# Performance work log

Measured on AMD Instinct MI355X. Metric: run time of the kernel, lower is better.

## Reference

```python
import jax, jax.numpy as jnp
import numpy as np

MODES = 256


def setup_inputs() -> dict:
    key = jax.random.key(0)
    k1, k2, k3, k4, k5 = jax.random.split(key, 5)
    B, C_IN, C_OUT, N, KM = 8, 128, 128, 8192, 32
    scale = 1.0 / (C_IN * C_OUT)
    return {
        "x": jax.random.normal(k1, (B, C_IN, N), dtype=jnp.float32),
        "wbases": jax.random.normal(k2, (B, N, MODES), dtype=jnp.float32),
        "bases": jax.random.normal(k3, (B, N, MODES), dtype=jnp.float32),
        "weights": scale * jax.random.normal(k4, (C_IN, C_OUT, KM), dtype=jnp.float32),
        "D": jax.random.normal(k5, (KM, MODES), dtype=jnp.float32),
    }


def reference(x, wbases, bases, weights, D):
    # Project onto weighted bases: (b, c_in, n) x (b, n, modes) -> (b, c_in, modes)
    x_hat = jnp.einsum('bcx,bxk->bck', x, wbases[:, :, :MODES])
    # D-weighted channel mixing. Original: x_hat1[b,i,j,k] = x_hat[b,i,k]*D[j,k];
    # y[b,o,k] = sum_{i,j} x_hat1[b,i,j,k] * weights[i,o,j]
    # Equivalent fused contraction (same math, no 4D broadcast):
    y_hat = jnp.einsum('bik,jk,ioj->bok', x_hat, D, weights)
    # Reconstruct on output bases: (b, c_out, modes) x (b, n, modes) -> (b, c_out, n)
    y = jnp.einsum('bck,bxk->bcx', y_hat, bases[:, :, :MODES])
    return y
```

## Files before the change

### kernel.cpp

```cpp
#include <hip/hip_runtime.h>

#define B_    8
#define CIN   128
#define COUT  128
#define NX    8192
#define KMJ   32
#define MODES 256

typedef short bf16x8 __attribute__((ext_vector_type(8)));
typedef float f32x4  __attribute__((ext_vector_type(4)));

__device__ __forceinline__ float bf2f(unsigned short u) {
    union { unsigned int i; float f; } v; v.i = ((unsigned int)u) << 16; return v.f;
}
__device__ __forceinline__ unsigned short f2bf(float f) {
    union { float f; unsigned int i; } v; v.f = f;
    unsigned int x = v.i;
    return (unsigned short)((x + 0x7fffu + ((x >> 16) & 1u)) >> 16);
}
__device__ __forceinline__ bf16x8 cvt8(const float* __restrict__ p) {
    f32x4 a = *(const f32x4*)p;
    f32x4 b = *(const f32x4*)(p + 4);
    bf16x8 r;
    r[0] = (short)f2bf(a[0]); r[1] = (short)f2bf(a[1]);
    r[2] = (short)f2bf(a[2]); r[3] = (short)f2bf(a[3]);
    r[4] = (short)f2bf(b[0]); r[5] = (short)f2bf(b[1]);
    r[6] = (short)f2bf(b[2]); r[7] = (short)f2bf(b[3]);
    return r;
}
__device__ __forceinline__ ushort4 cvt4(f32x4 a) {
    ushort4 r;
    r.x = f2bf(a[0]); r.y = f2bf(a[1]); r.z = f2bf(a[2]); r.w = f2bf(a[3]);
    return r;
}

__global__ __launch_bounds__(256) void k1_wk(const float* __restrict__ W,
                                             const float* __restrict__ D,
                                             unsigned short* __restrict__ Wk) {
    int wave = threadIdx.x >> 6, lane = threadIdx.x & 63;
    int quad = lane >> 4, l16 = lane & 15;
    int gw  = blockIdx.x * 4 + wave;
    int oi0 = gw * 16;
    int i0  = oi0 & 127, o0 = oi0 >> 7;
    bf16x8 bfrag = cvt8(W + ((size_t)(i0 + l16) * COUT + o0) * KMJ + quad * 8);
    for (int mt = 0; mt < 16; mt++) {
        int k0 = mt * 16;
        bf16x8 afrag;
#pragma unroll
        for (int jj = 0; jj < 8; jj++)
            afrag[jj] = (short)f2bf(D[(quad * 8 + jj) * MODES + k0 + l16]);
        f32x4 acc = {0.f, 0.f, 0.f, 0.f};
        acc = __builtin_amdgcn_mfma_f32_16x16x32_bf16(afrag, bfrag, acc, 0, 0, 0);
#pragma unroll
        for (int r = 0; r < 4; r++)
            Wk[(size_t)(k0 + quad * 4 + r) * (CIN * COUT) + oi0 + l16] = f2bf(acc[r]);
    }
}

__global__ __launch_bounds__(512) void k2_xhat(const float* __restrict__ X,
                                               const float* __restrict__ WB,
                                               unsigned short* __restrict__ PART) {
    __shared__ __align__(16) unsigned short Xs[128 * 40];
    __shared__ __align__(16) unsigned short WBs[32 * 260];
    int nt = blockIdx.x, b = blockIdx.y;
    int r0 = nt * 256;
    int t  = threadIdx.x;
    int wave = t >> 6, lane = t & 63;
    int wm = wave >> 2, wn = wave & 3;
    int quad = lane >> 4, l16 = lane & 15;

    const float* xb  = X  + (size_t)b * CIN * NX;
    const float* wbb = WB + (size_t)b * NX * MODES;

    int xn4 = t & 7,  xc  = t >> 3;
    int wk4 = t & 63, wn0 = t >> 6;

    f32x4 acc[4][4];
#pragma unroll
    for (int i = 0; i < 4; i++)
#pragma unroll
        for (int j = 0; j < 4; j++) acc[i][j] = (f32x4){0.f, 0.f, 0.f, 0.f};

    for (int s = 0; s < 8; s++) {
        int rs = r0 + s * 32;
        f32x4 xv0 = *(const f32x4*)(xb + (size_t)xc * NX + rs + xn4 * 4);
        f32x4 xv1 = *(const f32x4*)(xb + (size_t)(xc + 64) * NX + rs + xn4 * 4);
        f32x4 wv[4];
#pragma unroll
        for (int r = 0; r < 4; r++)
            wv[r] = *(const f32x4*)(wbb + (size_t)(rs + wn0 + 8 * r) * MODES + wk4 * 4);

        __syncthreads();
        *(ushort4*)(Xs + xc * 40 + xn4 * 4)        = cvt4(xv0);
        *(ushort4*)(Xs + (xc + 64) * 40 + xn4 * 4) = cvt4(xv1);
#pragma unroll
        for (int r = 0; r < 4; r++)
            *(ushort4*)(WBs + (wn0 + 8 * r) * 260 + wk4 * 4) = cvt4(wv[r]);
        __syncthreads();

        bf16x8 af[4];
#pragma unroll
        for (int tm = 0; tm < 4; tm++)
            af[tm] = *(const bf16x8*)(Xs + (wm * 64 + tm * 16 + l16) * 40 + quad * 8);
        bf16x8 bfv[4];
#pragma unroll
        for (int tn = 0; tn < 4; tn++) {
            int km = wn * 64 + tn * 16 + l16;
#pragma unroll
            for (int jj = 0; jj < 8; jj++)
                bfv[tn][jj] = (short)WBs[(quad * 8 + jj) * 260 + km];
        }
#pragma unroll
        for (int tm = 0; tm < 4; tm++)
#pragma unroll
            for (int tn = 0; tn < 4; tn++)
                acc[tm][tn] = __builtin_amdgcn_mfma_f32_16x16x32_bf16(af[tm], bfv[tn], acc[tm][tn], 0, 0, 0);
    }

    unsigned short* pb = PART + ((size_t)b * 32 + nt) * (CIN * MODES);
#pragma unroll
    for (int tm = 0; tm < 4; tm++) {
        int c = wm * 64 + tm * 16 + quad * 4;
#pragma unroll
        for (int tn = 0; tn < 4; tn++) {
            int km = wn * 64 + tn * 16 + l16;
#pragma unroll
            for (int r = 0; r < 4; r++)
                pb[(size_t)(c + r) * MODES + km] = f2bf(acc[tm][tn][r]);
        }
    }
}

__global__ __launch_bounds__(256) void k2b_red(const unsigned short* __restrict__ PART,
                                               float* __restrict__ XH) {
    int e0 = blockIdx.x * 1024 + threadIdx.x;
#pragma unroll
    for (int r = 0; r < 4; r++) {
        int e = e0 + r * 256;
        int b = e >> 15, rem = e & 32767;
        const unsigned short* p = PART + (size_t)b * 32 * (CIN * MODES) + rem;
        float acc = 0.f;
#pragma unroll
        for (int nt = 0; nt < 32; nt++) acc += bf2f(p[nt * (CIN * MODES)]);
        XH[e] = acc;
    }
}

__global__ __launch_bounds__(256) void k3_yhat(const float* __restrict__ XH,
                                               const unsigned short* __restrict__ Wk,
                                               unsigned short* __restrict__ YH) {
    __shared__ float xs[128][8];
    int k = blockIdx.x;
    int t = threadIdx.x;
#pragma unroll
    for (int l = 0; l < 4; l++) {
        int e = l * 256 + t;
        int i = e >> 3, b = e & 7;
        xs[i][b] = XH[(size_t)b * (CIN * MODES) + (size_t)i * MODES + k];
    }
    __syncthreads();
    int o = t & 127, bh = t >> 7;
    const unsigned short* wp = Wk + (size_t)k * (CIN * COUT) + (size_t)o * CIN;
    f32x4 acc = {0.f, 0.f, 0.f, 0.f};
    for (int ii = 0; ii < 16; ii++) {
        bf16x8 wc = *(const bf16x8*)(wp + ii * 8);
#pragma unroll
        for (int jj = 0; jj < 8; jj++) {
            float w = bf2f((unsigned short)wc[jj]);
            f32x4 xv = *(const f32x4*)&xs[ii * 8 + jj][bh * 4];
            acc += w * xv;
        }
    }
#pragma unroll
    for (int r = 0; r < 4; r++)
        YH[((size_t)(bh * 4 + r) * COUT + o) * MODES + k] = f2bf(acc[r]);
}

__global__ __launch_bounds__(256) void k4_y(const unsigned short* __restrict__ YH,
                                            const float* __restrict__ BA,
                                            float* __restrict__ Y) {
    __shared__ __align__(16) unsigned short As[128 * 32];
    __shared__ __align__(16) unsigned short Bs[128 * 32];
    int b  = blockIdx.y;
    int n0 = blockIdx.x * 128;
    int t  = threadIdx.x;
    int wave = t >> 6, lane = t & 63;
    int wm = wave >> 1, wn = wave & 1;
    int quad = lane >> 4, l16 = lane & 15;

    const unsigned short* yhb = YH + (size_t)b * COUT * MODES;
    const float* bab = BA + (size_t)b * NX * MODES + (size_t)n0 * MODES;

    int E0 = t * 8;
    int row0 = E0 >> 5, kk0 = E0 & 31;
    int row1 = (2048 + E0) >> 5, kk1 = (2048 + E0) & 31;

    f32x4 acc[4][4];
#pragma unroll
    for (int i = 0; i < 4; i++)
#pragma unroll
        for (int j = 0; j < 4; j++) acc[i][j] = (f32x4){0.f, 0.f, 0.f, 0.f};

    bf16x8 av0 = *(const bf16x8*)(yhb + (size_t)row0 * MODES + kk0);
    bf16x8 av1 = *(const bf16x8*)(yhb + (size_t)row1 * MODES + kk1);
    f32x4 bv0a = *(const f32x4*)(bab + (size_t)row0 * MODES + kk0);
    f32x4 bv0b = *(const f32x4*)(bab + (size_t)row0 * MODES + kk0 + 4);
    f32x4 bv1a = *(const f32x4*)(bab + (size_t)row1 * MODES + kk1);
    f32x4 bv1b = *(const f32x4*)(bab + (size_t)row1 * MODES + kk1 + 4);

    for (int step = 0; step < 8; step++) {
        __syncthreads();
        *(bf16x8*)(As + E0)        = av0;
        *(bf16x8*)(As + 2048 + E0) = av1;
        bf16x8 bs0, bs1;
        bs0[0]=(short)f2bf(bv0a[0]); bs0[1]=(short)f2bf(bv0a[1]);
        bs0[2]=(short)f2bf(bv0a[2]); bs0[3]=(short)f2bf(bv0a[3]);
        bs0[4]=(short)f2bf(bv0b[0]); bs0[5]=(short)f2bf(bv0b[1]);
        bs0[6]=(short)f2bf(bv0b[2]); bs0[7]=(short)f2bf(bv0b[3]);
        bs1[0]=(short)f2bf(bv1a[0]); bs1[1]=(short)f2bf(bv1a[1]);
        bs1[2]=(short)f2bf(bv1a[2]); bs1[3]=(short)f2bf(bv1a[3]);
        bs1[4]=(short)f2bf(bv1b[0]); bs1[5]=(short)f2bf(bv1b[1]);
        bs1[6]=(short)f2bf(bv1b[2]); bs1[7]=(short)f2bf(bv1b[3]);
        *(bf16x8*)(Bs + E0)        = bs0;
        *(bf16x8*)(Bs + 2048 + E0) = bs1;
        __syncthreads();

        if (step < 7) {
            int ks = (step + 1) * 32;
            av0  = *(const bf16x8*)(yhb + (size_t)row0 * MODES + ks + kk0);
            av1  = *(const bf16x8*)(yhb + (size_t)row1 * MODES + ks + kk1);
            bv0a = *(const f32x4*)(bab + (size_t)row0 * MODES + ks + kk0);
            bv0b = *(const f32x4*)(bab + (size_t)row0 * MODES + ks + kk0 + 4);
            bv1a = *(const f32x4*)(bab + (size_t)row1 * MODES + ks + kk1);
            bv1b = *(const f32x4*)(bab + (size_t)row1 * MODES + ks + kk1 + 4);
        }

        bf16x8 af[4], bfv[4];
#pragma unroll
        for (int tm = 0; tm < 4; tm++) {
            int c = wm * 64 + tm * 16 + l16;
            af[tm] = *(const bf16x8*)(As + c * 32 + quad * 8);
        }
#pragma unroll
        for (int tn = 0; tn < 4; tn++) {
            int n = wn * 64 + tn * 16 + l16;
            bfv[tn] = *(const bf16x8*)(Bs + n * 32 + quad * 8);
        }
#pragma unroll
        for (int tm = 0; tm < 4; tm++)
#pragma unroll
            for (int tn = 0; tn < 4; tn++)
                acc[tm][tn] = __builtin_amdgcn_mfma_f32_16x16x32_bf16(af[tm], bfv[tn], acc[tm][tn], 0, 0, 0);
    }

    float* yb = Y + (size_t)b * COUT * NX;
#pragma unroll
    for (int tm = 0; tm < 4; tm++) {
        int o = wm * 64 + tm * 16 + quad * 4;
#pragma unroll
        for (int tn = 0; tn < 4; tn++) {
            int n = n0 + wn * 64 + tn * 16 + l16;
#pragma unroll
            for (int r = 0; r < 4; r++)
                yb[(size_t)(o + r) * NX + n] = acc[tm][tn][r];
        }
    }
}

extern "C" void kernel_launch(void* const* d_in, const int* in_sizes, int n_in,
                              void* d_out, int out_size, void* d_ws, size_t ws_size,
                              hipStream_t stream) {
    const float* X  = (const float*)d_in[0];
    const float* WB = (const float*)d_in[1];
    const float* BA = (const float*)d_in[2];
    const float* W  = (const float*)d_in[3];
    const float* D  = (const float*)d_in[4];
    float* Y = (float*)d_out;

    char* ws = (char*)d_ws;
    unsigned short* Wk   = (unsigned short*)ws;
    float*          XH   = (float*)(ws + (8u << 20));
    unsigned short* YH   = (unsigned short*)(ws + (9u << 20));
    unsigned short* PART = (unsigned short*)(ws + (10u << 20));

    k1_wk  <<<256,          256, 0, stream>>>(W, D, Wk);
    k2_xhat<<<dim3(32, 8),  512, 0, stream>>>(X, WB, PART);
    k2b_red<<<256,          256, 0, stream>>>(PART, XH);
    k3_yhat<<<MODES,        256, 0, stream>>>(XH, Wk, YH);
    k4_y   <<<dim3(64, 8),  256, 0, stream>>>(YH, BA, Y);
}
```

Before: 221.0 us.

## Split x_hat kernel over mode halves, prefetch next tile, transpose WB in LDS

The projection kernel grid gains a third dimension that splits the 256 modes into two halves of 128. This doubles the block count from 256 to 512 for better CU occupancy, at the cost of each half re-reading x. Loads are now register-prefetched one stage ahead so global reads overlap the MFMA work, and thread roles are split between x loading and WB loading. WB is stored transposed in LDS so B fragments are read as single 16-byte vector loads instead of eight scalar strided reads.

```diff
diff --git a/kernel.cpp b/kernel.cpp
--- a/kernel.cpp
+++ b/kernel.cpp
@@ -57,70 +57,94 @@
     }
 }
 
-__global__ __launch_bounds__(512) void k2_xhat(const float* __restrict__ X,
-                                               const float* __restrict__ WB,
-                                               unsigned short* __restrict__ PART) {
+__global__ __launch_bounds__(512, 4) void k2_xhat(const float* __restrict__ X,
+                                                  const float* __restrict__ WB,
+                                                  unsigned short* __restrict__ PART) {
     __shared__ __align__(16) unsigned short Xs[128 * 40];
-    __shared__ __align__(16) unsigned short WBs[32 * 260];
-    int nt = blockIdx.x, b = blockIdx.y;
+    __shared__ __align__(16) unsigned short WBT[8 * 552];
+    int nt = blockIdx.x, b = blockIdx.y, kh = blockIdx.z;
     int r0 = nt * 256;
     int t  = threadIdx.x;
     int wave = t >> 6, lane = t & 63;
-    int wm = wave >> 2, wn = wave & 3;
+    int wm = wave >> 1, wn = wave & 1;
     int quad = lane >> 4, l16 = lane & 15;
 
     const float* xb  = X  + (size_t)b * CIN * NX;
-    const float* wbb = WB + (size_t)b * NX * MODES;
-
-    int xn4 = t & 7,  xc  = t >> 3;
-    int wk4 = t & 63, wn0 = t >> 6;
-
-    f32x4 acc[4][4];
-#pragma unroll
-    for (int i = 0; i < 4; i++)
+    const float* wbb = WB + (size_t)b * NX * MODES + kh * 128;
+
+    bool isX = (t >= 256);
+    int t2 = t & 255;
+    int xn4 = t2 & 7,  xc = t2 >> 3;
+    int kq  = t2 & 31, nq = t2 >> 5;
+
+    f32x4 acc[2][4];
+#pragma unroll
+    for (int i = 0; i < 2; i++)
 #pragma unroll
         for (int j = 0; j < 4; j++) acc[i][j] = (f32x4){0.f, 0.f, 0.f, 0.f};
 
+    f32x4 st[4];
+    if (isX) {
+#pragma unroll
+        for (int r = 0; r < 4; r++)
+            st[r] = *(const f32x4*)(xb + (size_t)(xc + 32 * r) * NX + r0 + 4 * xn4);
+    } else {
+#pragma unroll
+        for (int r = 0; r < 4; r++)
+            st[r] = *(const f32x4*)(wbb + (size_t)(r0 + 4 * nq + r) * MODES + 4 * kq);
+    }
+
     for (int s = 0; s < 8; s++) {
-        int rs = r0 + s * 32;
-        f32x4 xv0 = *(const f32x4*)(xb + (size_t)xc * NX + rs + xn4 * 4);
-        f32x4 xv1 = *(const f32x4*)(xb + (size_t)(xc + 64) * NX + rs + xn4 * 4);
-        f32x4 wv[4];
-#pragma unroll
-        for (int r = 0; r < 4; r++)
-            wv[r] = *(const f32x4*)(wbb + (size_t)(rs + wn0 + 8 * r) * MODES + wk4 * 4);
-
         __syncthreads();
-        *(ushort4*)(Xs + xc * 40 + xn4 * 4)        = cvt4(xv0);
-        *(ushort4*)(Xs + (xc + 64) * 40 + xn4 * 4) = cvt4(xv1);
-#pragma unroll
-        for (int r = 0; r < 4; r++)
-            *(ushort4*)(WBs + (wn0 + 8 * r) * 260 + wk4 * 4) = cvt4(wv[r]);
+        if (isX) {
+#pragma unroll
+            for (int r = 0; r < 4; r++)
+                *(ushort4*)(Xs + (xc + 32 * r) * 40 + 4 * xn4) = cvt4(st[r]);
+        } else {
+#pragma unroll
+            for (int j = 0; j < 4; j++) {
+                int k = 4 * kq + j;
+                ushort4 w;
+                w.x = f2bf(st[0][j]); w.y = f2bf(st[1][j]);
+                w.z = f2bf(st[2][j]); w.w = f2bf(st[3][j]);
+                *(ushort4*)(WBT + (k >> 4) * 552 + (k & 15) * 32 + ((k >> 2) & 3) * 8 + 4 * nq) = w;
+            }
+        }
         __syncthreads();
 
-        bf16x8 af[4];
-#pragma unroll
-        for (int tm = 0; tm < 4; tm++)
-            af[tm] = *(const bf16x8*)(Xs + (wm * 64 + tm * 16 + l16) * 40 + quad * 8);
-        bf16x8 bfv[4];
+        if (s < 7) {
+            int rs = r0 + (s + 1) * 32;
+            if (isX) {
+#pragma unroll
+                for (int r = 0; r < 4; r++)
+                    st[r] = *(const f32x4*)(xb + (size_t)(xc + 32 * r) * NX + rs + 4 * xn4);
+            } else {
+#pragma unroll
+                for (int r = 0; r < 4; r++)
+                    st[r] = *(const f32x4*)(wbb + (size_t)(rs + 4 * nq + r) * MODES + 4 * kq);
+            }
+        }
+
+        bf16x8 af[2], bfv[4];
+#pragma unroll
+        for (int tm = 0; tm < 2; tm++)
+            af[tm] = *(const bf16x8*)(Xs + (wm * 32 + tm * 16 + l16) * 40 + quad * 8);
 #pragma unroll
         for (int tn = 0; tn < 4; tn++) {
             int km = wn * 64 + tn * 16 + l16;
-#pragma unroll
-            for (int jj = 0; jj < 8; jj++)
-                bfv[tn][jj] = (short)WBs[(quad * 8 + jj) * 260 + km];
-        }
-#pragma unroll
-        for (int tm = 0; tm < 4; tm++)
+            bfv[tn] = *(const bf16x8*)(WBT + (km >> 4) * 552 + (km & 15) * 32 + ((km >> 2) & 3) * 8 + quad * 8);
+        }
+#pragma unroll
+        for (int tm = 0; tm < 2; tm++)
 #pragma unroll
             for (int tn = 0; tn < 4; tn++)
                 acc[tm][tn] = __builtin_amdgcn_mfma_f32_16x16x32_bf16(af[tm], bfv[tn], acc[tm][tn], 0, 0, 0);
     }
 
-    unsigned short* pb = PART + ((size_t)b * 32 + nt) * (CIN * MODES);
-#pragma unroll
-    for (int tm = 0; tm < 4; tm++) {
-        int c = wm * 64 + tm * 16 + quad * 4;
+    unsigned short* pb = PART + ((size_t)b * 32 + nt) * (CIN * MODES) + kh * 128;
+#pragma unroll
+    for (int tm = 0; tm < 2; tm++) {
+        int c = wm * 32 + tm * 16 + quad * 4;
 #pragma unroll
         for (int tn = 0; tn < 4; tn++) {
             int km = wn * 64 + tn * 16 + l16;
@@ -283,9 +307,9 @@
     unsigned short* YH   = (unsigned short*)(ws + (9u << 20));
     unsigned short* PART = (unsigned short*)(ws + (10u << 20));
 
-    k1_wk  <<<256,          256, 0, stream>>>(W, D, Wk);
-    k2_xhat<<<dim3(32, 8),  512, 0, stream>>>(X, WB, PART);
-    k2b_red<<<256,          256, 0, stream>>>(PART, XH);
-    k3_yhat<<<MODES,        256, 0, stream>>>(XH, Wk, YH);
-    k4_y   <<<dim3(64, 8),  256, 0, stream>>>(YH, BA, Y);
-}
+    k1_wk  <<<256,            256, 0, stream>>>(W, D, Wk);
+    k2_xhat<<<dim3(32, 8, 2), 512, 0, stream>>>(X, WB, PART);
+    k2b_red<<<256,            256, 0, stream>>>(PART, XH);
+    k3_yhat<<<MODES,          256, 0, stream>>>(XH, Wk, YH);
+    k4_y   <<<dim3(64, 8),    256, 0, stream>>>(YH, BA, Y);
+}
```

Measured after the change: 220.4 us. About the same (-0.3%).
